# Kernel tuning notes

Hardware: AMD Instinct MI355X
Metric: run time of the kernel (lower is better)

Reference implementation:

```python
import jax, jax.numpy as jnp
import numpy as np

N_BANKS = 16
BAND = 4
D = 32          # n_neurons_per_hidd_bank
N_IN = 3072     # n_input_neurons
N_OUT = 1000    # n_output_neurons
B = 8192        # batch size
IDX_INPUT = [0, 1]
IDX_OUTPUT = [14, 15]
# edge list (source, target), target-major, ascending sources per target --
# matches the torch loop order (np.where over bank_conn[:, i_target])
EDGES = [(s, t) for t in range(N_BANKS) for s in range(max(0, t - BAND), t)]
E = len(EDGES)  # 54
TGT_EDGES = [[e for e, (s, t) in enumerate(EDGES) if t == tt] for tt in range(N_BANKS)]
BN_EPS = 1e-5


def _bn(a):
    # BatchNorm1d in training mode: batch mean, biased batch variance
    m = a.mean(axis=0)
    v = a.var(axis=0)
    return (a - m) * jax.lax.rsqrt(v + BN_EPS)


def setup_inputs() -> dict:
    key = jax.random.key(0)
    ks = jax.random.split(key, 8)
    return {
        "x": jax.random.normal(ks[0], (B, N_IN), jnp.float32),
        "bn_gamma": jnp.ones((N_IN,), jnp.float32),
        "bn_beta": jnp.zeros((N_IN,), jnp.float32),
        "W_in": jax.random.normal(ks[1], (len(IDX_INPUT), N_IN, D), jnp.float32) / np.float32(np.sqrt(N_IN)),
        "b_in": jax.random.normal(ks[2], (len(IDX_INPUT), D), jnp.float32) / np.float32(np.sqrt(N_IN)),
        "Wg": jax.random.normal(ks[3], (E, D), jnp.float32) / np.float32(np.sqrt(D)),
        "Wd": jax.random.normal(ks[4], (E, D, D), jnp.float32) / np.float32(np.sqrt(D)),
        "bd": jax.random.normal(ks[5], (E, D), jnp.float32) / np.float32(np.sqrt(D)),
        "Wout": jax.random.normal(ks[6], (len(IDX_OUTPUT), D, N_OUT), jnp.float32) / np.float32(np.sqrt(D)),
    }


def reference(x, bn_gamma, bn_beta, W_in, b_in, Wg, Wd, bd, Wout):
    # input batch norm (affine)
    x = _bn(x) * bn_gamma + bn_beta
    acts = [None] * N_BANKS
    for k, i in enumerate(IDX_INPUT):
        acts[i] = jax.nn.relu(x @ W_in[k] + b_in[k])  # [B, D]
    total_gate = jnp.zeros((x.shape[0], 1), x.dtype)
    for t in range(N_BANKS):
        acc = acts[t]  # non-None only for input banks
        for e in TGT_EDGES[t]:
            s = EDGES[e][0]
            gate = jnp.clip(acts[s] @ Wg[e], 0.0, 1.0)[:, None]  # hardtanh(.,0,1), [B,1]
            total_gate = total_gate + gate
            data = acts[s] @ Wd[e] + bd[e]                       # [B, D]
            acc = gate * data if acc is None else acc + gate * data
        acts[t] = _bn(jax.nn.relu(acc))  # hidden batch norm, affine=False
    output = None
    for k, i in enumerate(IDX_OUTPUT):
        d = acts[i] @ Wout[k]  # Linear(D, N_OUT, bias=False)
        output = d if output is None else output + d
    return output, total_gate
```

## Files before the change

kernel.cpp:

```cpp
#include <hip/hip_runtime.h>


#define BATCH 8192
#define NIN 3072
#define DD 32
#define NB 16
#define NOUT 1000
#define TGOFF (BATCH * NOUT)
#define BNEPS 1e-5f

#define O_SUM 0
#define O_SUM2 3072
#define O_STATS2 6144
#define O_TG 22528
#define ZERO_FLOATS 30720
#define O_SCALE 30720
#define O_SHIFT 33792
#define O_BIAS 36864
#define O_BP 36928
#define O_ACTS 233536
#define O_ACC (O_ACTS + 2 * BATCH * DD)

__global__ void __launch_bounds__(256) k_stats(const float* __restrict__ x, float* __restrict__ ws) {
    int c = blockIdx.x * 256 + threadIdx.x;
    const float* p = x + (size_t)blockIdx.y * 256 * NIN + c;
    float s = 0.f, s2 = 0.f;
#pragma unroll 8
    for (int i = 0; i < 256; i++) { float v = p[(size_t)i * NIN]; s += v; s2 += v * v; }
    atomicAdd(&ws[O_SUM + c], s);
    atomicAdd(&ws[O_SUM2 + c], s2);
}

__global__ void __launch_bounds__(256) k_prep(float* __restrict__ ws, const float* __restrict__ g,
                                              const float* __restrict__ b, const float* __restrict__ b_in) {
    int c = blockIdx.x * 256 + threadIdx.x;
    float mean = ws[O_SUM + c] * (1.f / BATCH);
    float var = ws[O_SUM2 + c] * (1.f / BATCH) - mean * mean;
    float sc = g[c] * rsqrtf(fmaxf(var, 0.f) + BNEPS);
    ws[O_SCALE + c] = sc;
    ws[O_SHIFT + c] = b[c] - mean * sc;
    if (c < 64) ws[O_BIAS + c] = b_in[c];
}

__global__ void __launch_bounds__(256) k_bias(float* __restrict__ ws, const float* __restrict__ W_in) {
    int bank = blockIdx.x & 1, jc = blockIdx.x >> 1;
    int d = threadIdx.x & 31, js = threadIdx.x >> 5;
    int j0 = jc * 256 + js * 32;
    float a = 0.f;
    for (int j = 0; j < 32; j++)
        a += ws[O_SHIFT + j0 + j] * W_in[(size_t)bank * NIN * DD + (size_t)(j0 + j) * DD + d];
    __shared__ float red[8][32];
    red[js][d] = a;
    __syncthreads();
    if (threadIdx.x < 32) {
        float t = 0.f;
#pragma unroll
        for (int g8 = 0; g8 < 8; g8++) t += red[g8][threadIdx.x];
        atomicAdd(&ws[O_BIAS + bank * 32 + threadIdx.x], t);
    }
}

__global__ void __launch_bounds__(256) k_bfold(float* __restrict__ ws, const float* __restrict__ W_in) {
    int idx = blockIdx.x * 256 + threadIdx.x;
    int j = idx >> 6, c = idx & 63;
    ws[O_BP + idx] = ws[O_SCALE + j] * W_in[(size_t)(c >> 5) * NIN * DD + (size_t)j * DD + (c & 31)];
}

__global__ void __launch_bounds__(256) k_gemm3(const float* __restrict__ x, float* __restrict__ ws) {
    __shared__ float xL[64][20];
    __shared__ float bL[16][64];
    int tid = threadIdx.x;
    int row0 = blockIdx.x * 64;
    int k00 = blockIdx.y * 768;
    const float* bp = ws + O_BP;
    float acc[4][4] = {};
    int tx = tid & 15, rt = tid >> 4;
    int lr = tid >> 2, lq = tid & 3;
    int br = tid >> 4, bq = tid & 15;
    for (int kc = 0; kc < 48; kc++) {
        int k0 = k00 + kc * 16;
        float4 xv = *(const float4*)&x[(size_t)(row0 + lr) * NIN + k0 + lq * 4];
        float4 bv = *(const float4*)&bp[(size_t)(k0 + br) * 64 + bq * 4];
        __syncthreads();
        *(float4*)&xL[lr][lq * 4] = xv;
        *(float4*)&bL[br][bq * 4] = bv;
        __syncthreads();
#pragma unroll
        for (int kk = 0; kk < 16; kk += 4) {
            float4 b0 = *(float4*)&bL[kk][tx * 4];
            float4 b1 = *(float4*)&bL[kk + 1][tx * 4];
            float4 b2 = *(float4*)&bL[kk + 2][tx * 4];
            float4 b3 = *(float4*)&bL[kk + 3][tx * 4];
#pragma unroll
            for (int j = 0; j < 4; j++) {
                float4 xv4 = *(float4*)&xL[rt * 4 + j][kk];
                acc[j][0] += xv4.x * b0.x + xv4.y * b1.x + xv4.z * b2.x + xv4.w * b3.x;
                acc[j][1] += xv4.x * b0.y + xv4.y * b1.y + xv4.z * b2.y + xv4.w * b3.y;
                acc[j][2] += xv4.x * b0.z + xv4.y * b1.z + xv4.z * b2.z + xv4.w * b3.z;
                acc[j][3] += xv4.x * b0.w + xv4.y * b1.w + xv4.z * b2.w + xv4.w * b3.w;
            }
        }
    }
    float* dst = ws + O_ACC + (size_t)blockIdx.y * (BATCH * 64);
#pragma unroll
    for (int j = 0; j < 4; j++) {
        float4 v = make_float4(acc[j][0], acc[j][1], acc[j][2], acc[j][3]);
        *(float4*)&dst[(size_t)(row0 + rt * 4 + j) * 64 + tx * 4] = v;
    }
}

__global__ void __launch_bounds__(256) k_act(float* __restrict__ ws) {
    int i4 = (blockIdx.x * 256 + threadIdx.x) * 4;
    const float* ac = ws + O_ACC;
    float4 s0 = *(const float4*)&ac[i4];
    float4 s1 = *(const float4*)&ac[524288 + i4];
    float4 s2 = *(const float4*)&ac[1048576 + i4];
    float4 s3 = *(const float4*)&ac[1572864 + i4];
    int c = i4 & 63, row = i4 >> 6;
    const float* bias = ws + O_BIAS;
    float4 v;
    v.x = fmaxf(s0.x + s1.x + s2.x + s3.x + bias[c], 0.f);
    v.y = fmaxf(s0.y + s1.y + s2.y + s3.y + bias[c + 1], 0.f);
    v.z = fmaxf(s0.z + s1.z + s2.z + s3.z + bias[c + 2], 0.f);
    v.w = fmaxf(s0.w + s1.w + s2.w + s3.w + bias[c + 3], 0.f);
    int bank = c >> 5, dd = c & 31;
    *(float4*)&ws[O_ACTS + ((size_t)bank * BATCH + row) * DD + dd] = v;
}

__global__ void __launch_bounds__(256) k_bank(int t, float* __restrict__ ws,
                                              const float* __restrict__ Wg, const float* __restrict__ Wd,
                                              const float* __restrict__ bd) {
    __shared__ float asrcL[4][8][32];
    __shared__ float WdL[4][1024];
    __shared__ float mML[4][32], ivL[4][32];
    __shared__ float red[8][64];
    int tid = threadIdx.x;
    int rg = tid >> 5, d = tid & 31;
    int row0 = blockIdx.x * 8;
    int slot = blockIdx.x & 15;
    float* acts = ws + O_ACTS;
    float* stats = ws + O_STATS2;
    int nE = t < 4 ? t : 4;
    int s0 = t - nE;
    int eb = (t <= 4) ? t * (t - 1) / 2 : 10 + 4 * (t - 5);
    for (int p = tid; p < nE * 256; p += 256)
        ((float4*)&WdL[0][0])[p] = ((const float4*)(Wd + (size_t)eb * 1024))[p];
    float wgr[4], bdr[4];
#pragma unroll
    for (int ei = 0; ei < 4; ei++) {
        wgr[ei] = (ei < nE) ? Wg[(eb + ei) * 32 + d] : 0.f;
        bdr[ei] = (ei < nE) ? bd[(eb + ei) * 32 + d] : 0.f;
    }
    if (tid < nE * 32) {
        int si = tid >> 5, dd = tid & 31;
        const float* st = stats + (size_t)(s0 + si) * 16 * 64;
        float sm = 0.f, sq = 0.f;
#pragma unroll
        for (int sl = 0; sl < 16; sl++) { sm += st[sl * 64 + dd]; sq += st[sl * 64 + 32 + dd]; }
        float m = sm * (1.f / BATCH);
        float var = sq * (1.f / BATCH) - m * m;
        mML[si][dd] = m;
        ivL[si][dd] = rsqrtf(fmaxf(var, 0.f) + BNEPS);
    }
    float cur = (t < 2) ? acts[((size_t)t * BATCH + row0 + rg) * DD + d] : 0.f;
    __syncthreads();
#pragma unroll 4
    for (int si = 0; si < nE; si++)
        asrcL[si][rg][d] = (acts[((size_t)(s0 + si) * BATCH + row0 + rg) * DD + d] - mML[si][d]) * ivL[si][d];
    __syncthreads();
    float tg = 0.f;
#pragma unroll
    for (int ei = 0; ei < 4; ei++) {
        if (ei < nE) {
            float g = asrcL[ei][rg][d] * wgr[ei];
            g += __shfl_xor(g, 1); g += __shfl_xor(g, 2); g += __shfl_xor(g, 4);
            g += __shfl_xor(g, 8); g += __shfl_xor(g, 16);
            g = fminf(fmaxf(g, 0.f), 1.f);
            tg += g;
            float dat = bdr[ei];
            const float* ar = asrcL[ei][rg];
            const float* wc = &WdL[ei][d];
#pragma unroll
            for (int k = 0; k < 32; k += 4) {
                float4 a4 = *(const float4*)&ar[k];
                dat += a4.x * wc[k * 32] + a4.y * wc[(k + 1) * 32]
                     + a4.z * wc[(k + 2) * 32] + a4.w * wc[(k + 3) * 32];
            }
            cur += g * dat;
        }
    }
    float v = fmaxf(cur, 0.f);
    acts[((size_t)t * BATCH + row0 + rg) * DD + d] = v;
    if (d == 0 && nE > 0) ws[O_TG + row0 + rg] += tg;
    red[rg][d] = v; red[rg][32 + d] = v * v;
    __syncthreads();
    if (tid < 64) {
        float a = 0.f;
#pragma unroll
        for (int g8 = 0; g8 < 8; g8++) a += red[g8][tid];
        atomicAdd(&stats[((size_t)t * 16 + slot) * 64 + tid], a);
    }
}

__global__ void __launch_bounds__(256) k_out(const float* __restrict__ ws, const float* __restrict__ Wout,
                                             float* __restrict__ out) {
    __shared__ float aLt[32][68];
    __shared__ float wL[32][128];
    __shared__ float mIv[2][2][32];
    int tid = threadIdx.x;
    int row0 = blockIdx.x * 64;
    int col0 = blockIdx.y * 128;
    const float* acts = ws + O_ACTS;
    if (blockIdx.y == 0 && tid < 64) out[TGOFF + row0 + tid] = ws[O_TG + row0 + tid];
    if (tid < 64) {
        int bi = tid >> 5, d = tid & 31;
        const float* st = ws + O_STATS2 + (size_t)(14 + bi) * 16 * 64;
        float sm = 0.f, sq = 0.f;
#pragma unroll
        for (int sl = 0; sl < 16; sl++) { sm += st[sl * 64 + d]; sq += st[sl * 64 + 32 + d]; }
        float m = sm * (1.f / BATCH);
        float var = sq * (1.f / BATCH) - m * m;
        mIv[bi][0][d] = m;
        mIv[bi][1][d] = rsqrtf(fmaxf(var, 0.f) + BNEPS);
    }
    int tx = tid & 31, ty = tid >> 5;
    int c4 = col0 + tx * 4;
    bool c4ok = (c4 + 3 < NOUT);
    float acc[8][4] = {};
    for (int bi = 0; bi < 2; bi++) {
        __syncthreads();
        {
            int d = tid & 31, r0 = tid >> 5;
            float m = mIv[bi][0][d], iv = mIv[bi][1][d];
            const float* ap = acts + ((size_t)(14 + bi) * BATCH + row0) * DD + d;
#pragma unroll
            for (int i = 0; i < 8; i++) {
                int r = r0 + 8 * i;
                aLt[d][r] = (ap[(size_t)r * DD] - m) * iv;
            }
        }
        {
            const float* wp = Wout + (size_t)bi * DD * NOUT + c4;
            int kk0 = tid >> 5;
#pragma unroll
            for (int i = 0; i < 4; i++) {
                int kk = kk0 + 8 * i;
                const float* wr = wp + (size_t)kk * NOUT;
                float4 v;
                if (c4ok) {
                    v = *(const float4*)wr;
                } else {
                    v.x = (c4 + 0 < NOUT) ? wr[0] : 0.f;
                    v.y = (c4 + 1 < NOUT) ? wr[1] : 0.f;
                    v.z = (c4 + 2 < NOUT) ? wr[2] : 0.f;
                    v.w = (c4 + 3 < NOUT) ? wr[3] : 0.f;
                }
                *(float4*)&wL[kk][tx * 4] = v;
            }
        }
        __syncthreads();
#pragma unroll 4
        for (int k = 0; k < 32; k++) {
            float4 w = *(float4*)&wL[k][tx * 4];
            float4 a0 = *(float4*)&aLt[k][ty * 8];
            float4 a1 = *(float4*)&aLt[k][ty * 8 + 4];
            float ar[8] = {a0.x, a0.y, a0.z, a0.w, a1.x, a1.y, a1.z, a1.w};
            float wc[4] = {w.x, w.y, w.z, w.w};
#pragma unroll
            for (int r = 0; r < 8; r++)
#pragma unroll
                for (int c = 0; c < 4; c++)
                    acc[r][c] += ar[r] * wc[c];
        }
    }
    if (c4ok) {
#pragma unroll
        for (int r = 0; r < 8; r++) {
            int row = row0 + ty * 8 + r;
            *(float4*)&out[(size_t)row * NOUT + c4] =
                make_float4(acc[r][0], acc[r][1], acc[r][2], acc[r][3]);
        }
    } else {
#pragma unroll
        for (int r = 0; r < 8; r++) {
            int row = row0 + ty * 8 + r;
#pragma unroll
            for (int c = 0; c < 4; c++)
                if (c4 + c < NOUT) out[(size_t)row * NOUT + c4 + c] = acc[r][c];
        }
    }
}

extern "C" void kernel_launch(void* const* d_in, const int* in_sizes, int n_in,
                              void* d_out, int out_size, void* d_ws, size_t ws_size,
                              hipStream_t stream) {
    (void)in_sizes; (void)n_in; (void)out_size; (void)ws_size;
    const float* x     = (const float*)d_in[0];
    const float* gamma = (const float*)d_in[1];
    const float* beta  = (const float*)d_in[2];
    const float* W_in  = (const float*)d_in[3];
    const float* b_in  = (const float*)d_in[4];
    const float* Wg    = (const float*)d_in[5];
    const float* Wd    = (const float*)d_in[6];
    const float* bd    = (const float*)d_in[7];
    const float* Wout  = (const float*)d_in[8];
    float* out = (float*)d_out;
    float* ws  = (float*)d_ws;

    hipMemsetAsync(d_ws, 0, ZERO_FLOATS * sizeof(float), stream);
    k_stats<<<dim3(12, 32), 256, 0, stream>>>(x, ws);
    k_prep<<<12, 256, 0, stream>>>(ws, gamma, beta, b_in);
    k_bias<<<24, 256, 0, stream>>>(ws, W_in);
    k_bfold<<<768, 256, 0, stream>>>(ws, W_in);
    k_gemm3<<<dim3(128, 4), 256, 0, stream>>>(x, ws);
    k_act<<<512, 256, 0, stream>>>(ws);
    for (int t = 0; t < NB; t++)
        k_bank<<<1024, 256, 0, stream>>>(t, ws, Wg, Wd, bd);
    k_out<<<dim3(128, 8), 256, 0, stream>>>(ws, Wout, out);
}
```

Measured before the change: 409.7 us.

## Fuse per-bank launches into one persistent kernel with grid-wide flag barriers

Replaces the sixteen k_bank launches with a single persistent kernel of 512 blocks, each owning 16 rows. Bank activations stay in a shared-memory ring, and the next bank's Wd is double-buffered. Blocks synchronise on global atomic flag counters before reading the previous bank's BN statistics, and k_act now also accumulates bank-0 stats. It also doubles k_stats grid parallelism. This removes launch overhead and global round-trips of activations, but relies on all 512 blocks being co-resident to avoid deadlock, and the flags alias the O_SUM region.

```diff
diff --git a/kernel.cpp b/kernel.cpp
--- a/kernel.cpp
+++ b/kernel.cpp
@@ -8,8 +8,11 @@
 #define NOUT 1000
 #define TGOFF (BATCH * NOUT)
 #define BNEPS 1e-5f
+#define NBLK 512
+#define ROWS 16
 
 #define O_SUM 0
+#define O_FLAG 0
 #define O_SUM2 3072
 #define O_STATS2 6144
 #define O_TG 22528
@@ -23,10 +26,10 @@
 
 __global__ void __launch_bounds__(256) k_stats(const float* __restrict__ x, float* __restrict__ ws) {
     int c = blockIdx.x * 256 + threadIdx.x;
-    const float* p = x + (size_t)blockIdx.y * 256 * NIN + c;
+    const float* p = x + (size_t)blockIdx.y * 128 * NIN + c;
     float s = 0.f, s2 = 0.f;
 #pragma unroll 8
-    for (int i = 0; i < 256; i++) { float v = p[(size_t)i * NIN]; s += v; s2 += v * v; }
+    for (int i = 0; i < 128; i++) { float v = p[(size_t)i * NIN]; s += v; s2 += v * v; }
     atomicAdd(&ws[O_SUM + c], s);
     atomicAdd(&ws[O_SUM2 + c], s2);
 }
@@ -110,7 +113,10 @@
 }
 
 __global__ void __launch_bounds__(256) k_act(float* __restrict__ ws) {
-    int i4 = (blockIdx.x * 256 + threadIdx.x) * 4;
+    __shared__ float sred[16][32];
+    __shared__ float qred[16][32];
+    int tid = threadIdx.x;
+    int i4 = (blockIdx.x * 256 + tid) * 4;
     const float* ac = ws + O_ACC;
     float4 s0 = *(const float4*)&ac[i4];
     float4 s1 = *(const float4*)&ac[524288 + i4];
@@ -125,80 +131,162 @@
     v.w = fmaxf(s0.w + s1.w + s2.w + s3.w + bias[c + 3], 0.f);
     int bank = c >> 5, dd = c & 31;
     *(float4*)&ws[O_ACTS + ((size_t)bank * BATCH + row) * DD + dd] = v;
-}
-
-__global__ void __launch_bounds__(256) k_bank(int t, float* __restrict__ ws,
-                                              const float* __restrict__ Wg, const float* __restrict__ Wd,
-                                              const float* __restrict__ bd) {
-    __shared__ float asrcL[4][8][32];
-    __shared__ float WdL[4][1024];
-    __shared__ float mML[4][32], ivL[4][32];
+    int r16 = tid >> 4;
+    if (bank == 0) {
+        *(float4*)&sred[r16][dd] = v;
+        *(float4*)&qred[r16][dd] = make_float4(v.x * v.x, v.y * v.y, v.z * v.z, v.w * v.w);
+    }
+    __syncthreads();
+    if (tid < 32) {
+        float sm = 0.f, sq = 0.f;
+#pragma unroll
+        for (int r = 0; r < 16; r++) { sm += sred[r][tid]; sq += qred[r][tid]; }
+        int slot = blockIdx.x & 15;
+        float* st = ws + O_STATS2 + (size_t)slot * 64;
+        atomicAdd(&st[tid], sm);
+        atomicAdd(&st[32 + tid], sq);
+    }
+}
+
+__global__ void __launch_bounds__(256, 2) k_banks(float* __restrict__ ws,
+                                                  const float* __restrict__ Wg,
+                                                  const float* __restrict__ Wd,
+                                                  const float* __restrict__ bd) {
+    __shared__ float ring[4][ROWS][32];
+    __shared__ float asrcL[4][ROWS][32];
+    __shared__ float WdL[2][4][1024];
+    __shared__ float mL[4][32], ivL[4][32];
     __shared__ float red[8][64];
     int tid = threadIdx.x;
     int rg = tid >> 5, d = tid & 31;
-    int row0 = blockIdx.x * 8;
+    int row0 = blockIdx.x * ROWS;
     int slot = blockIdx.x & 15;
     float* acts = ws + O_ACTS;
     float* stats = ws + O_STATS2;
-    int nE = t < 4 ? t : 4;
-    int s0 = t - nE;
-    int eb = (t <= 4) ? t * (t - 1) / 2 : 10 + 4 * (t - 5);
-    for (int p = tid; p < nE * 256; p += 256)
-        ((float4*)&WdL[0][0])[p] = ((const float4*)(Wd + (size_t)eb * 1024))[p];
-    float wgr[4], bdr[4];
-#pragma unroll
-    for (int ei = 0; ei < 4; ei++) {
-        wgr[ei] = (ei < nE) ? Wg[(eb + ei) * 32 + d] : 0.f;
-        bdr[ei] = (ei < nE) ? bd[(eb + ei) * 32 + d] : 0.f;
-    }
-    if (tid < nE * 32) {
-        int si = tid >> 5, dd = tid & 31;
-        const float* st = stats + (size_t)(s0 + si) * 16 * 64;
+    int* flag = (int*)(ws + O_FLAG);
+    float tg[2] = {0.f, 0.f};
+    float cur[2];
+#pragma unroll
+    for (int ri = 0; ri < 2; ri++) {
+        int r = rg + 8 * ri;
+        ring[0][r][d] = acts[(size_t)(row0 + r) * DD + d];
+        cur[ri] = acts[((size_t)BATCH + row0 + r) * DD + d];
+    }
+    if (tid < 32) {
+        const float* st = stats;
         float sm = 0.f, sq = 0.f;
 #pragma unroll
-        for (int sl = 0; sl < 16; sl++) { sm += st[sl * 64 + dd]; sq += st[sl * 64 + 32 + dd]; }
+        for (int sl = 0; sl < 16; sl++) { sm += st[sl * 64 + tid]; sq += st[sl * 64 + 32 + tid]; }
         float m = sm * (1.f / BATCH);
         float var = sq * (1.f / BATCH) - m * m;
-        mML[si][dd] = m;
-        ivL[si][dd] = rsqrtf(fmaxf(var, 0.f) + BNEPS);
-    }
-    float cur = (t < 2) ? acts[((size_t)t * BATCH + row0 + rg) * DD + d] : 0.f;
-    __syncthreads();
-#pragma unroll 4
-    for (int si = 0; si < nE; si++)
-        asrcL[si][rg][d] = (acts[((size_t)(s0 + si) * BATCH + row0 + rg) * DD + d] - mML[si][d]) * ivL[si][d];
-    __syncthreads();
-    float tg = 0.f;
-#pragma unroll
-    for (int ei = 0; ei < 4; ei++) {
-        if (ei < nE) {
-            float g = asrcL[ei][rg][d] * wgr[ei];
-            g += __shfl_xor(g, 1); g += __shfl_xor(g, 2); g += __shfl_xor(g, 4);
-            g += __shfl_xor(g, 8); g += __shfl_xor(g, 16);
-            g = fminf(fmaxf(g, 0.f), 1.f);
-            tg += g;
-            float dat = bdr[ei];
-            const float* ar = asrcL[ei][rg];
-            const float* wc = &WdL[ei][d];
-#pragma unroll
-            for (int k = 0; k < 32; k += 4) {
-                float4 a4 = *(const float4*)&ar[k];
-                dat += a4.x * wc[k * 32] + a4.y * wc[(k + 1) * 32]
-                     + a4.z * wc[(k + 2) * 32] + a4.w * wc[(k + 3) * 32];
-            }
-            cur += g * dat;
-        }
-    }
-    float v = fmaxf(cur, 0.f);
-    acts[((size_t)t * BATCH + row0 + rg) * DD + d] = v;
-    if (d == 0 && nE > 0) ws[O_TG + row0 + rg] += tg;
-    red[rg][d] = v; red[rg][32 + d] = v * v;
-    __syncthreads();
-    if (tid < 64) {
-        float a = 0.f;
-#pragma unroll
-        for (int g8 = 0; g8 < 8; g8++) a += red[g8][tid];
-        atomicAdd(&stats[((size_t)t * 16 + slot) * 64 + tid], a);
+        mL[0][tid] = m;
+        ivL[0][tid] = rsqrtf(fmaxf(var, 0.f) + BNEPS);
+    }
+    if (tid < 256) {
+        ((float4*)&WdL[1][0][0])[tid] = ((const float4*)Wd)[tid];
+    }
+    for (int t = 1; t < 16; t++) {
+        int buf = t & 1;
+        int nE = t < 4 ? t : 4;
+        int s0 = t - nE;
+        int eb = (t <= 4) ? t * (t - 1) / 2 : 10 + 4 * (t - 5);
+        if (t < 15) {
+            int t2 = t + 1;
+            int nE2 = t2 < 4 ? t2 : 4;
+            int eb2 = (t2 <= 4) ? t2 * (t2 - 1) / 2 : 10 + 4 * (t2 - 5);
+            for (int p = tid; p < nE2 * 256; p += 256)
+                ((float4*)&WdL[buf ^ 1][0][0])[p] = ((const float4*)(Wd + (size_t)eb2 * 1024))[p];
+        }
+        float wgr[4], bdr[4];
+#pragma unroll
+        for (int ei = 0; ei < 4; ei++) {
+            wgr[ei] = (ei < nE) ? Wg[(eb + ei) * 32 + d] : 0.f;
+            bdr[ei] = (ei < nE) ? bd[(eb + ei) * 32 + d] : 0.f;
+        }
+        if (t > 1) {
+            if (tid == 0) {
+                while (__hip_atomic_load(&flag[t - 1], __ATOMIC_RELAXED, __HIP_MEMORY_SCOPE_AGENT) < NBLK)
+                    __builtin_amdgcn_s_sleep(2);
+            }
+            __syncthreads();
+            if (tid < 32) {
+                const float* st = stats + (size_t)(t - 1) * 16 * 64;
+                float sm = 0.f, sq = 0.f;
+#pragma unroll
+                for (int sl = 0; sl < 16; sl++) {
+                    sm += __hip_atomic_load(&st[sl * 64 + tid], __ATOMIC_RELAXED, __HIP_MEMORY_SCOPE_AGENT);
+                    sq += __hip_atomic_load(&st[sl * 64 + 32 + tid], __ATOMIC_RELAXED, __HIP_MEMORY_SCOPE_AGENT);
+                }
+                float m = sm * (1.f / BATCH);
+                float var = sq * (1.f / BATCH) - m * m;
+                mL[(t - 1) & 3][tid] = m;
+                ivL[(t - 1) & 3][tid] = rsqrtf(fmaxf(var, 0.f) + BNEPS);
+            }
+        }
+        __syncthreads();
+#pragma unroll
+        for (int si = 0; si < 4; si++) {
+            if (si < nE) {
+                int sl4 = (s0 + si) & 3;
+#pragma unroll
+                for (int ri = 0; ri < 2; ri++) {
+                    int r = rg + 8 * ri;
+                    asrcL[si][r][d] = (ring[sl4][r][d] - mL[sl4][d]) * ivL[sl4][d];
+                }
+            }
+        }
+        __syncthreads();
+        float vv[2];
+#pragma unroll
+        for (int ri = 0; ri < 2; ri++) {
+            int r = rg + 8 * ri;
+            float c = (t == 1) ? cur[ri] : 0.f;
+#pragma unroll
+            for (int ei = 0; ei < 4; ei++) {
+                if (ei < nE) {
+                    float g = asrcL[ei][r][d] * wgr[ei];
+                    g += __shfl_xor(g, 1); g += __shfl_xor(g, 2); g += __shfl_xor(g, 4);
+                    g += __shfl_xor(g, 8); g += __shfl_xor(g, 16);
+                    g = fminf(fmaxf(g, 0.f), 1.f);
+                    tg[ri] += g;
+                    float dat = bdr[ei];
+                    const float* ar = asrcL[ei][r];
+                    const float* wc = &WdL[buf][ei][d];
+#pragma unroll
+                    for (int k = 0; k < 32; k += 4) {
+                        float4 a4 = *(const float4*)&ar[k];
+                        dat += a4.x * wc[k * 32] + a4.y * wc[(k + 1) * 32]
+                             + a4.z * wc[(k + 2) * 32] + a4.w * wc[(k + 3) * 32];
+                    }
+                    c += g * dat;
+                }
+            }
+            vv[ri] = fmaxf(c, 0.f);
+        }
+        __syncthreads();
+#pragma unroll
+        for (int ri = 0; ri < 2; ri++) {
+            int r = rg + 8 * ri;
+            ring[t & 3][r][d] = vv[ri];
+            if (t >= 14) acts[((size_t)t * BATCH + row0 + r) * DD + d] = vv[ri];
+        }
+        red[rg][d] = vv[0] + vv[1];
+        red[rg][32 + d] = vv[0] * vv[0] + vv[1] * vv[1];
+        __syncthreads();
+        if (tid < 64) {
+            float a = 0.f;
+#pragma unroll
+            for (int g8 = 0; g8 < 8; g8++) a += red[g8][tid];
+            atomicAdd(&stats[((size_t)t * 16 + slot) * 64 + tid], a);
+        }
+        if (t < 15) {
+            __syncthreads();
+            if (tid == 0) atomicAdd(&flag[t], 1);
+        }
+    }
+    if (d == 0) {
+        ws[O_TG + row0 + rg] = tg[0];
+        ws[O_TG + row0 + rg + 8] = tg[1];
     }
 }
 
@@ -308,13 +396,13 @@
     float* ws  = (float*)d_ws;
 
     hipMemsetAsync(d_ws, 0, ZERO_FLOATS * sizeof(float), stream);
-    k_stats<<<dim3(12, 32), 256, 0, stream>>>(x, ws);
+    k_stats<<<dim3(12, 64), 256, 0, stream>>>(x, ws);
     k_prep<<<12, 256, 0, stream>>>(ws, gamma, beta, b_in);
     k_bias<<<24, 256, 0, stream>>>(ws, W_in);
     k_bfold<<<768, 256, 0, stream>>>(ws, W_in);
     k_gemm3<<<dim3(128, 4), 256, 0, stream>>>(x, ws);
     k_act<<<512, 256, 0, stream>>>(ws);
-    for (int t = 0; t < NB; t++)
-        k_bank<<<1024, 256, 0, stream>>>(t, ws, Wg, Wd, bd);
+    hipMemsetAsync(ws + O_FLAG, 0, 16 * sizeof(int), stream);
+    k_banks<<<NBLK, 256, 0, stream>>>(ws, Wg, Wd, bd);
     k_out<<<dim3(128, 8), 256, 0, stream>>>(ws, Wout, out);
 }
```

Result: slower. 433.0 us (+5.7%).
